# Optimization experiments

Hardware: AMD Instinct MI355X
Metric: run time of the kernel (lower is better)

## Reference

```python
import jax, jax.numpy as jnp
import numpy as np

DIM = 1024
NUM_HEADS = 16
HEAD_DIM = DIM // NUM_HEADS
SCALE = HEAD_DIM ** -0.5


def setup_inputs() -> dict:
    key = jax.random.key(0)
    ks = jax.random.split(key, 9)
    s = 1.0 / np.sqrt(DIM)
    x = jax.random.normal(ks[0], (2, 2048, DIM), dtype=jnp.float32)
    Wq = jax.random.normal(ks[1], (DIM, DIM), dtype=jnp.float32) * s
    Wk = jax.random.normal(ks[2], (DIM, DIM), dtype=jnp.float32) * s
    Wv = jax.random.normal(ks[3], (DIM, DIM), dtype=jnp.float32) * s
    Wp = jax.random.normal(ks[4], (DIM, DIM), dtype=jnp.float32) * s
    bq = jax.random.normal(ks[5], (DIM,), dtype=jnp.float32) * s
    bk = jax.random.normal(ks[6], (DIM,), dtype=jnp.float32) * s
    bv = jax.random.normal(ks[7], (DIM,), dtype=jnp.float32) * s
    bp = jax.random.normal(ks[8], (DIM,), dtype=jnp.float32) * s
    return {"x": x, "Wq": Wq, "bq": bq, "Wk": Wk, "bk": bk,
            "Wv": Wv, "bv": bv, "Wp": Wp, "bp": bp}


def reference(x, Wq, bq, Wk, bk, Wv, bv, Wp, bp):
    B, L, C = x.shape
    H, D = NUM_HEADS, HEAD_DIM
    # Linear projections (torch Linear: x @ W.T + b)
    q = x @ Wq.T + bq
    k = x @ Wk.T + bk
    v = x @ Wv.T + bv
    # (B, L, H*D) -> (B, H, L, D)
    q = q.reshape(B, L, H, D).transpose(0, 2, 1, 3)
    k = k.reshape(B, L, H, D).transpose(0, 2, 1, 3)
    v = v.reshape(B, L, H, D).transpose(0, 2, 1, 3)
    # scaled dot-product attention, full L x L scores (as in source)
    attn = jnp.einsum('bhqd,bhkd->bhqk', q, k) * SCALE
    attn = jax.nn.softmax(attn, axis=-1)
    out = jnp.einsum('bhqk,bhkd->bhqd', attn, v)
    out = out.transpose(0, 2, 1, 3).reshape(B, L, C)
    return out @ Wp.T + bp
```

## Files before the change

kernel.cpp:

```cpp
#include <hip/hip_runtime.h>

#define DIMC 1024
#define SEQL 2048
#define NB   2
#define NH   16
#define HD   64
#define MTOT (NB*SEQL)
#define XSTR 2048
static constexpr float SM_SCALE = 0.125f;
static constexpr float LOG2E    = 1.4426950408889634f;
static constexpr float QSCALE   = SM_SCALE * LOG2E;

typedef short s16x8 __attribute__((ext_vector_type(8)));
typedef short s16x4 __attribute__((ext_vector_type(4)));
typedef float f32x4 __attribute__((ext_vector_type(4)));

__device__ __forceinline__ unsigned short f2bf(float f) {
    unsigned int u = __float_as_uint(f);
    u += 0x7fffu + ((u >> 16) & 1u);
    return (unsigned short)(u >> 16);
}
__device__ __forceinline__ s16x8 ld8(const unsigned short* p) {
    return *(const s16x8*)p;
}
__device__ __forceinline__ void gld_lds16(const unsigned short* g, unsigned short* l) {
    __builtin_amdgcn_global_load_lds(
        (const __attribute__((address_space(1))) void*)g,
        (__attribute__((address_space(3))) void*)l, 16, 0, 0);
}

__global__ __launch_bounds__(256) void cast_all(
    const float* __restrict__ x,
    const float* __restrict__ Wq, const float* __restrict__ Wk,
    const float* __restrict__ Wv, const float* __restrict__ Wp,
    const float* __restrict__ bq, const float* __restrict__ bk,
    const float* __restrict__ bvv,
    unsigned short* __restrict__ xb, unsigned short* __restrict__ wall,
    float* __restrict__ ball)
{
    const int bid = blockIdx.x, tid = threadIdx.x;
    if (bid < 4096) {
        int i = bid * 256 + tid;
        float4 f = ((const float4*)x)[i];
        s16x4 o;
        o[0] = (short)f2bf(f.x); o[1] = (short)f2bf(f.y);
        o[2] = (short)f2bf(f.z); o[3] = (short)f2bf(f.w);
        ((s16x4*)xb)[i] = o;
    } else if (bid < 8192) {
        int j = (bid - 4096) * 256 + tid;
        int r = j >> 18;
        const float* src = (r == 0) ? Wq : (r == 1) ? Wk : (r == 2) ? Wv : Wp;
        float4 f = ((const float4*)src)[j & 262143];
        s16x4 o;
        o[0] = (short)f2bf(f.x); o[1] = (short)f2bf(f.y);
        o[2] = (short)f2bf(f.z); o[3] = (short)f2bf(f.w);
        ((s16x4*)wall)[j] = o;
    } else {
        int t2 = (bid - 8192) * 256 + tid;
        if (t2 < 3072)
            ball[t2] = (t2 < 1024) ? bq[t2]
                     : (t2 < 2048) ? bk[t2 - 1024] : bvv[t2 - 2048];
    }
}

__global__ __launch_bounds__(256) void gemm_tile(
    const unsigned short* __restrict__ A, int astride,
    const unsigned short* __restrict__ Wb,
    const float* __restrict__ bias,
    unsigned short* qk, unsigned short* vtb, float* outf, int mode)
{
    __shared__ __align__(16) unsigned short Asm[128 * 32];
    __shared__ __align__(16) unsigned short Bsm[128 * 32];

    const int t    = threadIdx.x;
    const int lane = t & 63;
    const int l15  = lane & 15;
    const int quad = lane >> 4;
    const int w    = t >> 6;
    const int mrow = (w & 1) * 64;
    const int ncol = (w >> 1) * 64;
    const int mt   = blockIdx.x & 31;
    const int nt   = blockIdx.x >> 5;
    const int row0 = mt * 128;

    const unsigned short* ga = A  + (size_t)(row0 + (t >> 2)) * astride + (t & 3) * 8;
    const unsigned short* gb = Wb + (size_t)(nt * 128 + (t >> 2)) * DIMC + (t & 3) * 8;
    const size_t gaStep = (size_t)64 * astride;
    const size_t gbStep = (size_t)64 * DIMC;

    f32x4 acc[4][4] = {};

    for (int k0 = 0; k0 < DIMC; k0 += 32) {
        gld_lds16(ga + k0,          Asm + t * 8);
        gld_lds16(ga + gaStep + k0, Asm + 2048 + t * 8);
        gld_lds16(gb + k0,          Bsm + t * 8);
        gld_lds16(gb + gbStep + k0, Bsm + 2048 + t * 8);
        __syncthreads();

        s16x8 a[4], b[4];
#pragma unroll
        for (int mi = 0; mi < 4; ++mi)
            a[mi] = *(const s16x8*)(Asm + (mrow + mi * 16 + l15) * 32 + quad * 8);
#pragma unroll
        for (int ni = 0; ni < 4; ++ni)
            b[ni] = *(const s16x8*)(Bsm + (ncol + ni * 16 + l15) * 32 + quad * 8);
#pragma unroll
        for (int mi = 0; mi < 4; ++mi)
#pragma unroll
            for (int ni = 0; ni < 4; ++ni)
                acc[mi][ni] = __builtin_amdgcn_mfma_f32_16x16x32_bf16(
                    a[mi], b[ni], acc[mi][ni], 0, 0, 0);
        __syncthreads();
    }

    const int proj = nt >> 3;
#pragma unroll
    for (int ni = 0; ni < 4; ++ni) {
        const int cq = (nt & 7) * 128 + ncol + ni * 16 + l15;
        const float bz = bias[proj * 1024 + cq];
#pragma unroll
        for (int mi = 0; mi < 4; ++mi) {
            const int rbase = row0 + mrow + mi * 16 + quad * 4;
            if (mode == 0) {
                if (proj < 2) {
                    const float scale = (proj == 0) ? QSCALE : 1.0f;
#pragma unroll
                    for (int r = 0; r < 4; ++r)
                        qk[(size_t)(rbase + r) * XSTR + proj * DIMC + cq] =
                            f2bf((acc[mi][ni][r] + bz) * scale);
                } else {
                    const int h = cq >> 6, d = cq & 63;
                    const int bb = rbase >> 11, ll = rbase & (SEQL - 1);
                    s16x4 v4;
                    v4[0] = (short)f2bf(acc[mi][ni][0] + bz);
                    v4[1] = (short)f2bf(acc[mi][ni][1] + bz);
                    v4[2] = (short)f2bf(acc[mi][ni][2] + bz);
                    v4[3] = (short)f2bf(acc[mi][ni][3] + bz);
                    *(s16x4*)(vtb + ((size_t)((bb * NH + h) * HD + d)) * SEQL + ll) = v4;
                }
            } else {
#pragma unroll
                for (int r = 0; r < 4; ++r)
                    outf[(size_t)(rbase + r) * DIMC + cq] = acc[mi][ni][r] + bz;
            }
        }
    }
}

__global__ __launch_bounds__(256) void attn_fused(
    unsigned short* xqk,
    const unsigned short* __restrict__ vt)
{
    __shared__ __align__(16) unsigned short Ksm[64 * 64];
    __shared__ __align__(16) unsigned short Vsm[64 * 64];

    const int t    = threadIdx.x;
    const int lane = t & 63;
    const int l15  = lane & 15;
    const int quad = lane >> 4;
    const int w    = t >> 6;

    const int bh = blockIdx.x >> 4;
    const int qb = blockIdx.x & 15;
    const int h  = bh & (NH - 1);
    const int bb = bh >> 4;
    const int q0A = qb * 128 + w * 16;
    const int q0B = q0A + 64;

    unsigned short* qbase = xqk + (size_t)(bb * SEQL) * XSTR + h * HD + quad * 8;
    unsigned short* qrA = qbase + (size_t)(q0A + l15) * XSTR;
    unsigned short* qrB = qbase + (size_t)(q0B + l15) * XSTR;
    const s16x8 bqA0 = ld8(qrA), bqA1 = ld8(qrA + 32);
    const s16x8 bqB0 = ld8(qrB), bqB1 = ld8(qrB + 32);

    const int tr = t >> 3, tp = t & 7;
    const int swz = (tp ^ (tr & 7)) * 8;
    const unsigned short* kg = xqk + (size_t)bb * SEQL * XSTR + DIMC + h * HD
                               + (size_t)tr * XSTR + swz;
    const unsigned short* vg0 = vt + (size_t)(bh * HD + tr) * SEQL + swz;
    const unsigned short* vg1 = vt + (size_t)(bh * HD + 32 + tr) * SEQL + swz;

    f32x4 oA[4] = {}, oB[4] = {};
    float lsA = 0.f, lsB = 0.f;
    const int xk = l15 & 7;

    for (int j0 = 0; j0 < SEQL; j0 += 64) {
        gld_lds16(kg + (size_t)j0 * XSTR,        Ksm + t * 8);
        gld_lds16(kg + (size_t)(j0 + 32) * XSTR, Ksm + 2048 + t * 8);
        gld_lds16(vg0 + j0, Vsm + t * 8);
        gld_lds16(vg1 + j0, Vsm + 2048 + t * 8);
        __syncthreads();

#pragma unroll
        for (int hf = 0; hf < 2; ++hf) {
            const int k0 = (hf * 32 + l15) * 64;
            const int k1 = (hf * 32 + 16 + l15) * 64;
            s16x8 a00 = *(const s16x8*)(Ksm + k0 + ((quad       ^ xk) * 8));
            s16x8 a01 = *(const s16x8*)(Ksm + k0 + (((quad + 4) ^ xk) * 8));
            s16x8 a10 = *(const s16x8*)(Ksm + k1 + ((quad       ^ xk) * 8));
            s16x8 a11 = *(const s16x8*)(Ksm + k1 + (((quad + 4) ^ xk) * 8));

            s16x8 bv[4];
#pragma unroll
            for (int c = 0; c < 4; ++c) {
                const unsigned short* va = Vsm + (c * 16 + l15) * 64 + (quad & 1) * 4;
                const int kc0 = hf * 4 + (quad >> 1);
                s16x4 v0 = *(const s16x4*)(va + ((kc0       ^ xk) * 8));
                s16x4 v1 = *(const s16x4*)(va + (((kc0 + 2) ^ xk) * 8));
                bv[c][0] = v0[0]; bv[c][1] = v0[1]; bv[c][2] = v0[2]; bv[c][3] = v0[3];
                bv[c][4] = v1[0]; bv[c][5] = v1[1]; bv[c][6] = v1[2]; bv[c][7] = v1[3];
            }

            {
                f32x4 st0 = {}, st1 = {};
                st0 = __builtin_amdgcn_mfma_f32_16x16x32_bf16(a00, bqA0, st0, 0, 0, 0);
                st0 = __builtin_amdgcn_mfma_f32_16x16x32_bf16(a01, bqA1, st0, 0, 0, 0);
                st1 = __builtin_amdgcn_mfma_f32_16x16x32_bf16(a10, bqA0, st1, 0, 0, 0);
                st1 = __builtin_amdgcn_mfma_f32_16x16x32_bf16(a11, bqA1, st1, 0, 0, 0);
                s16x8 ap;
#pragma unroll
                for (int r = 0; r < 4; ++r) {
                    float p0 = exp2f(st0[r]);
                    float p1 = exp2f(st1[r]);
                    lsA += p0 + p1;
                    ap[r]     = (short)f2bf(p0);
                    ap[r + 4] = (short)f2bf(p1);
                }
#pragma unroll
                for (int c = 0; c < 4; ++c)
                    oA[c] = __builtin_amdgcn_mfma_f32_16x16x32_bf16(ap, bv[c], oA[c], 0, 0, 0);
            }
            {
                f32x4 st0 = {}, st1 = {};
                st0 = __builtin_amdgcn_mfma_f32_16x16x32_bf16(a00, bqB0, st0, 0, 0, 0);
                st0 = __builtin_amdgcn_mfma_f32_16x16x32_bf16(a01, bqB1, st0, 0, 0, 0);
                st1 = __builtin_amdgcn_mfma_f32_16x16x32_bf16(a10, bqB0, st1, 0, 0, 0);
                st1 = __builtin_amdgcn_mfma_f32_16x16x32_bf16(a11, bqB1, st1, 0, 0, 0);
                s16x8 ap;
#pragma unroll
                for (int r = 0; r < 4; ++r) {
                    float p0 = exp2f(st0[r]);
                    float p1 = exp2f(st1[r]);
                    lsB += p0 + p1;
                    ap[r]     = (short)f2bf(p0);
                    ap[r + 4] = (short)f2bf(p1);
                }
#pragma unroll
                for (int c = 0; c < 4; ++c)
                    oB[c] = __builtin_amdgcn_mfma_f32_16x16x32_bf16(ap, bv[c], oB[c], 0, 0, 0);
            }
        }
        __syncthreads();
    }

    lsA += __shfl_xor(lsA, 16);  lsA += __shfl_xor(lsA, 32);
    lsB += __shfl_xor(lsB, 16);  lsB += __shfl_xor(lsB, 32);

    float liA[4], liB[4];
#pragma unroll
    for (int r = 0; r < 4; ++r) {
        liA[r] = 1.0f / __shfl(lsA, quad * 4 + r, 64);
        liB[r] = 1.0f / __shfl(lsB, quad * 4 + r, 64);
    }

#pragma unroll
    for (int c = 0; c < 4; ++c) {
        const int d = c * 16 + l15;
#pragma unroll
        for (int r = 0; r < 4; ++r) {
            const int qr = quad * 4 + r;
            xqk[(size_t)(bb * SEQL + q0A + qr) * XSTR + h * HD + d] = f2bf(oA[c][r] * liA[r]);
            xqk[(size_t)(bb * SEQL + q0B + qr) * XSTR + h * HD + d] = f2bf(oB[c][r] * liB[r]);
        }
    }
}

extern "C" void kernel_launch(void* const* d_in, const int* in_sizes, int n_in,
                              void* d_out, int out_size, void* d_ws, size_t ws_size,
                              hipStream_t stream) {
    const float* x  = (const float*)d_in[0];
    const float* Wq = (const float*)d_in[1];
    const float* bq = (const float*)d_in[2];
    const float* Wk = (const float*)d_in[3];
    const float* bk = (const float*)d_in[4];
    const float* Wv = (const float*)d_in[5];
    const float* bv = (const float*)d_in[6];
    const float* Wp = (const float*)d_in[7];
    const float* bp = (const float*)d_in[8];
    float* out = (float*)d_out;
    unsigned short* vtb = (unsigned short*)d_out;
    unsigned short* xqk = (unsigned short*)d_in[0];

    unsigned short* ws   = (unsigned short*)d_ws;
    const size_t XELT = (size_t)MTOT * DIMC;
    const size_t WELT = (size_t)DIMC * DIMC;
    unsigned short* xb   = ws;
    unsigned short* wall = ws + XELT;
    float*          ball = (float*)(ws + 2 * XELT);

    cast_all<<<8204, 256, 0, stream>>>(x, Wq, Wk, Wv, Wp, bq, bk, bv, xb, wall, ball);

    gemm_tile<<<768, 256, 0, stream>>>(xb, DIMC, wall, ball, xqk, vtb, nullptr, 0);

    attn_fused<<<NB * NH * (SEQL / 128), 256, 0, stream>>>(xqk, vtb);

    gemm_tile<<<256, 256, 0, stream>>>(xqk, XSTR, wall + 3 * WELT, bp,
                                       nullptr, nullptr, out, 1);
}
```

Baseline: 234.8 us.

## Double-buffer K/V tiles in attention and truncate P to bf16 cheaply

Attention now keeps two LDS buffers for K and V and prefetches the next 64-key tile with global_load_lds while the current tile is computed, aiming to hide global load latency. Probabilities are converted to bf16 by masking off the low bits (truncation) instead of round-to-nearest, and pairs are packed with shifts and ORs; the row sum uses the truncated values so numerator and denominator stay consistent. The V fragment assembly uses a shufflevector. The loop still has a single __syncthreads per iteration, and that barrier is now placed after the prefetch into the other buffer is issued. This leaves a possible race on the buffer being overwritten and an unclear wait on the async loads, and it doubles LDS use.

After: 231.9 us. No clear change (-1.2%).

```diff
diff --git a/kernel.cpp b/kernel.cpp
--- a/kernel.cpp
+++ b/kernel.cpp
@@ -14,6 +14,7 @@
 typedef short s16x8 __attribute__((ext_vector_type(8)));
 typedef short s16x4 __attribute__((ext_vector_type(4)));
 typedef float f32x4 __attribute__((ext_vector_type(4)));
+typedef int   i32x4 __attribute__((ext_vector_type(4)));
 
 __device__ __forceinline__ unsigned short f2bf(float f) {
     unsigned int u = __float_as_uint(f);
@@ -151,8 +152,8 @@
     unsigned short* xqk,
     const unsigned short* __restrict__ vt)
 {
-    __shared__ __align__(16) unsigned short Ksm[64 * 64];
-    __shared__ __align__(16) unsigned short Vsm[64 * 64];
+    __shared__ __align__(16) unsigned short Ksm[2][64 * 64];
+    __shared__ __align__(16) unsigned short Vsm[2][64 * 64];
 
     const int t    = threadIdx.x;
     const int lane = t & 63;
@@ -184,31 +185,41 @@
     float lsA = 0.f, lsB = 0.f;
     const int xk = l15 & 7;
 
+    gld_lds16(kg,                    Ksm[0] + t * 8);
+    gld_lds16(kg + (size_t)32 * XSTR, Ksm[0] + 2048 + t * 8);
+    gld_lds16(vg0,                   Vsm[0] + t * 8);
+    gld_lds16(vg1,                   Vsm[0] + 2048 + t * 8);
+    __syncthreads();
+
     for (int j0 = 0; j0 < SEQL; j0 += 64) {
-        gld_lds16(kg + (size_t)j0 * XSTR,        Ksm + t * 8);
-        gld_lds16(kg + (size_t)(j0 + 32) * XSTR, Ksm + 2048 + t * 8);
-        gld_lds16(vg0 + j0, Vsm + t * 8);
-        gld_lds16(vg1 + j0, Vsm + 2048 + t * 8);
-        __syncthreads();
+        const int cur = (j0 >> 6) & 1, nxt = cur ^ 1;
+        if (j0 + 64 < SEQL) {
+            const int jn = j0 + 64;
+            gld_lds16(kg + (size_t)jn * XSTR,        Ksm[nxt] + t * 8);
+            gld_lds16(kg + (size_t)(jn + 32) * XSTR, Ksm[nxt] + 2048 + t * 8);
+            gld_lds16(vg0 + jn,                      Vsm[nxt] + t * 8);
+            gld_lds16(vg1 + jn,                      Vsm[nxt] + 2048 + t * 8);
+        }
+        const unsigned short* Kc = Ksm[cur];
+        const unsigned short* Vc = Vsm[cur];
 
 #pragma unroll
         for (int hf = 0; hf < 2; ++hf) {
             const int k0 = (hf * 32 + l15) * 64;
             const int k1 = (hf * 32 + 16 + l15) * 64;
-            s16x8 a00 = *(const s16x8*)(Ksm + k0 + ((quad       ^ xk) * 8));
-            s16x8 a01 = *(const s16x8*)(Ksm + k0 + (((quad + 4) ^ xk) * 8));
-            s16x8 a10 = *(const s16x8*)(Ksm + k1 + ((quad       ^ xk) * 8));
-            s16x8 a11 = *(const s16x8*)(Ksm + k1 + (((quad + 4) ^ xk) * 8));
+            s16x8 a00 = *(const s16x8*)(Kc + k0 + ((quad       ^ xk) * 8));
+            s16x8 a01 = *(const s16x8*)(Kc + k0 + (((quad + 4) ^ xk) * 8));
+            s16x8 a10 = *(const s16x8*)(Kc + k1 + ((quad       ^ xk) * 8));
+            s16x8 a11 = *(const s16x8*)(Kc + k1 + (((quad + 4) ^ xk) * 8));
 
             s16x8 bv[4];
 #pragma unroll
             for (int c = 0; c < 4; ++c) {
-                const unsigned short* va = Vsm + (c * 16 + l15) * 64 + (quad & 1) * 4;
+                const unsigned short* va = Vc + (c * 16 + l15) * 64 + (quad & 1) * 4;
                 const int kc0 = hf * 4 + (quad >> 1);
                 s16x4 v0 = *(const s16x4*)(va + ((kc0       ^ xk) * 8));
                 s16x4 v1 = *(const s16x4*)(va + (((kc0 + 2) ^ xk) * 8));
-                bv[c][0] = v0[0]; bv[c][1] = v0[1]; bv[c][2] = v0[2]; bv[c][3] = v0[3];
-                bv[c][4] = v1[0]; bv[c][5] = v1[1]; bv[c][6] = v1[2]; bv[c][7] = v1[3];
+                bv[c] = __builtin_shufflevector(v0, v1, 0, 1, 2, 3, 4, 5, 6, 7);
             }
 
             {
@@ -217,15 +228,19 @@
                 st0 = __builtin_amdgcn_mfma_f32_16x16x32_bf16(a01, bqA1, st0, 0, 0, 0);
                 st1 = __builtin_amdgcn_mfma_f32_16x16x32_bf16(a10, bqA0, st1, 0, 0, 0);
                 st1 = __builtin_amdgcn_mfma_f32_16x16x32_bf16(a11, bqA1, st1, 0, 0, 0);
-                s16x8 ap;
+                unsigned int t0[4], t1[4];
 #pragma unroll
                 for (int r = 0; r < 4; ++r) {
-                    float p0 = exp2f(st0[r]);
-                    float p1 = exp2f(st1[r]);
-                    lsA += p0 + p1;
-                    ap[r]     = (short)f2bf(p0);
-                    ap[r + 4] = (short)f2bf(p1);
+                    t0[r] = __float_as_uint(exp2f(st0[r])) & 0xffff0000u;
+                    t1[r] = __float_as_uint(exp2f(st1[r])) & 0xffff0000u;
+                    lsA += __uint_as_float(t0[r]) + __uint_as_float(t1[r]);
                 }
+                i32x4 api;
+                api[0] = (int)((t0[0] >> 16) | t0[1]);
+                api[1] = (int)((t0[2] >> 16) | t0[3]);
+                api[2] = (int)((t1[0] >> 16) | t1[1]);
+                api[3] = (int)((t1[2] >> 16) | t1[3]);
+                s16x8 ap = __builtin_bit_cast(s16x8, api);
 #pragma unroll
                 for (int c = 0; c < 4; ++c)
                     oA[c] = __builtin_amdgcn_mfma_f32_16x16x32_bf16(ap, bv[c], oA[c], 0, 0, 0);
@@ -236,15 +251,19 @@
                 st0 = __builtin_amdgcn_mfma_f32_16x16x32_bf16(a01, bqB1, st0, 0, 0, 0);
                 st1 = __builtin_amdgcn_mfma_f32_16x16x32_bf16(a10, bqB0, st1, 0, 0, 0);
                 st1 = __builtin_amdgcn_mfma_f32_16x16x32_bf16(a11, bqB1, st1, 0, 0, 0);
-                s16x8 ap;
+                unsigned int t0[4], t1[4];
 #pragma unroll
                 for (int r = 0; r < 4; ++r) {
-                    float p0 = exp2f(st0[r]);
-                    float p1 = exp2f(st1[r]);
-                    lsB += p0 + p1;
-                    ap[r]     = (short)f2bf(p0);
-                    ap[r + 4] = (short)f2bf(p1);
+                    t0[r] = __float_as_uint(exp2f(st0[r])) & 0xffff0000u;
+                    t1[r] = __float_as_uint(exp2f(st1[r])) & 0xffff0000u;
+                    lsB += __uint_as_float(t0[r]) + __uint_as_float(t1[r]);
                 }
+                i32x4 api;
+                api[0] = (int)((t0[0] >> 16) | t0[1]);
+                api[1] = (int)((t0[2] >> 16) | t0[3]);
+                api[2] = (int)((t1[0] >> 16) | t1[1]);
+                api[3] = (int)((t1[2] >> 16) | t1[3]);
+                s16x8 ap = __builtin_bit_cast(s16x8, api);
 #pragma unroll
                 for (int c = 0; c < 4; ++c)
                     oB[c] = __builtin_amdgcn_mfma_f32_16x16x32_bf16(ap, bv[c], oB[c], 0, 0, 0);
```
